# Optimization experiments

Measured on AMD Instinct MI355X. Metric: run time of the kernel, lower is better.

Reference implementation:

```python
import jax, jax.numpy as jnp
import numpy as np

IN_FEATURES = 1024
OUT_FEATURES = 64
KERNEL_DIMS = 16
N = 512


def setup_inputs() -> dict:
    key = jax.random.key(0)
    kx, kT = jax.random.split(key)
    x = jax.random.normal(kx, (N, IN_FEATURES), dtype=jnp.float32)
    T = jax.random.normal(kT, (IN_FEATURES, OUT_FEATURES, KERNEL_DIMS), dtype=jnp.float32)
    return {"x": x, "T": T}


def reference(x, T):
    n = x.shape[0]
    # Project: [N, in] @ [in, out*kd] -> [N, out, kd]
    matrices = (x @ T.reshape(T.shape[0], -1)).reshape(n, OUT_FEATURES, KERNEL_DIMS)
    # Pairwise L1 distance over kernel dims: [N, N, out]
    norm = jnp.abs(matrices[None, :, :, :] - matrices[:, None, :, :]).sum(axis=3)
    expnorm = jnp.exp(-norm)
    # Exclude self-similarity (diagonal) and sum over the batch axis
    mask = 1.0 - jnp.eye(n, dtype=x.dtype)
    o_b = (expnorm * mask[:, :, None]).sum(axis=1)  # [N, out]
    return jnp.concatenate([x, o_b], axis=1)
```

## Files before the change

### kernel.cpp

```cpp
#include <hip/hip_runtime.h>
#include <hip/hip_bf16.h>

#define NB     512
#define INF    1024
#define OUTF   64
#define KD     16
#define PROJ   (OUTF*KD)
#define OROW   (INF + OUTF)

typedef short short8 __attribute__((ext_vector_type(8)));
typedef float floatx4 __attribute__((ext_vector_type(4)));

__device__ __forceinline__ unsigned short f2bf(float f) {
    union { float f; unsigned u; } v; v.f = f;
    const unsigned u = v.u;
    return (unsigned short)((u + 0x7FFF + ((u >> 16) & 1)) >> 16);
}

__global__ __launch_bounds__(256) void copy_init(const float* __restrict__ x,
                                                 float* __restrict__ out) {
    const int row = blockIdx.x;
    const int t   = threadIdx.x;
    ((float4*)(out + (size_t)row * OROW))[t] =
        ((const float4*)(x + (size_t)row * INF))[t];
    if (t < 16) {
        ((float4*)(out + (size_t)row * OROW + INF))[t] =
            make_float4(-1.f, -1.f, -1.f, -1.f);
    }
}

#define LDT 40

__global__ __launch_bounds__(256) void gemm_mfma(const float* __restrict__ A,
                                                 const float* __restrict__ B,
                                                 float* __restrict__ C) {
    __shared__ short As[32 * LDT];
    __shared__ short Bs[64 * LDT];

    const int t    = threadIdx.x;
    const int lane = t & 63, w = t >> 6;
    const int bm = blockIdx.y * 32, bn = blockIdx.x * 64;
    const int mh = w & 1, nh = w >> 1;

    const int am = t >> 3, ak = (t & 7) * 4;
    const int bk = (t >> 4) * 2, bn0 = (t & 15) * 4;

    floatx4 acc0 = {0.f, 0.f, 0.f, 0.f};
    floatx4 acc1 = {0.f, 0.f, 0.f, 0.f};

    const int q = lane >> 4, c = lane & 15;
    const short* apf  = &As[(mh * 16 + c) * LDT + q * 8];
    const short* bpf0 = &Bs[(nh * 32 + c) * LDT + q * 8];
    const short* bpf1 = &Bs[(nh * 32 + 16 + c) * LDT + q * 8];

    for (int k0 = 0; k0 < INF; k0 += 32) {
        const float4 av  = *(const float4*)&A[(size_t)(bm + am) * INF + k0 + ak];
        const float4 bv0 = *(const float4*)&B[(size_t)(k0 + bk) * PROJ + bn + bn0];
        const float4 bv1 = *(const float4*)&B[(size_t)(k0 + bk + 1) * PROJ + bn + bn0];

        __syncthreads();
        const unsigned pa0 = f2bf(av.x) | ((unsigned)f2bf(av.y) << 16);
        const unsigned pa1 = f2bf(av.z) | ((unsigned)f2bf(av.w) << 16);
        *(uint2*)&As[am * LDT + ak] = make_uint2(pa0, pa1);
        *(unsigned*)&Bs[(bn0 + 0) * LDT + bk] = f2bf(bv0.x) | ((unsigned)f2bf(bv1.x) << 16);
        *(unsigned*)&Bs[(bn0 + 1) * LDT + bk] = f2bf(bv0.y) | ((unsigned)f2bf(bv1.y) << 16);
        *(unsigned*)&Bs[(bn0 + 2) * LDT + bk] = f2bf(bv0.z) | ((unsigned)f2bf(bv1.z) << 16);
        *(unsigned*)&Bs[(bn0 + 3) * LDT + bk] = f2bf(bv0.w) | ((unsigned)f2bf(bv1.w) << 16);
        __syncthreads();

        const short8 af  = *(const short8*)apf;
        const short8 bf0 = *(const short8*)bpf0;
        const short8 bf1 = *(const short8*)bpf1;
        acc0 = __builtin_amdgcn_mfma_f32_16x16x32_bf16(af, bf0, acc0, 0, 0, 0);
        acc1 = __builtin_amdgcn_mfma_f32_16x16x32_bf16(af, bf1, acc1, 0, 0, 0);
    }

#pragma unroll
    for (int r = 0; r < 4; ++r) {
        const int row = bm + mh * 16 + q * 4 + r;
        C[(size_t)row * PROJ + bn + nh * 32 + c]      = acc0[r];
        C[(size_t)row * PROJ + bn + nh * 32 + 16 + c] = acc1[r];
    }
}

__global__ __launch_bounds__(128) void pairwise_l1(const float* __restrict__ M,
                                                   float* __restrict__ out) {
    __shared__ float Mj[64 * 64];

    const int t  = threadIdx.x;
    const int o  = t & 3;
    const int il = t >> 2;
    const int og = blockIdx.x;
    const int ig = blockIdx.y;
    const int j0 = blockIdx.z * 64;
    const int i  = ig * 32 + il;

    const float4* myp = (const float4*)&M[(size_t)i * PROJ + og * 64 + o * 16];
    const float4 a0 = myp[0], a1 = myp[1], a2 = myp[2], a3 = myp[3];

#pragma unroll
    for (int cc = 0; cc < 8; ++cc) {
        const int idx = (cc * 128 + t) * 4;
        const int jl  = idx >> 6;
        const int col = idx & 63;
        *(float4*)&Mj[jl * 64 + col] =
            *(const float4*)&M[(size_t)(j0 + jl) * PROJ + og * 64 + col];
    }
    __syncthreads();

    float sum0 = 0.f, sum1 = 0.f;
#pragma unroll 4
    for (int jl = 0; jl < 64; ++jl) {
        const float4* bp = (const float4*)&Mj[jl * 64 + o * 16];
        const float4 b0 = bp[0], b1 = bp[1], b2 = bp[2], b3 = bp[3];
        float n0 = fabsf(a0.x - b0.x) + fabsf(a0.y - b0.y) +
                   fabsf(a0.z - b0.z) + fabsf(a0.w - b0.w);
        float n1 = fabsf(a1.x - b1.x) + fabsf(a1.y - b1.y) +
                   fabsf(a1.z - b1.z) + fabsf(a1.w - b1.w);
        float n2 = fabsf(a2.x - b2.x) + fabsf(a2.y - b2.y) +
                   fabsf(a2.z - b2.z) + fabsf(a2.w - b2.w);
        float n3 = fabsf(a3.x - b3.x) + fabsf(a3.y - b3.y) +
                   fabsf(a3.z - b3.z) + fabsf(a3.w - b3.w);
        const float norm = (n0 + n1) + (n2 + n3);
        if (jl & 1) sum1 += __expf(-norm);
        else        sum0 += __expf(-norm);
    }

    __hip_atomic_fetch_add(&out[(size_t)i * OROW + INF + og * 4 + o],
                           sum0 + sum1, __ATOMIC_RELAXED,
                           __HIP_MEMORY_SCOPE_AGENT);
}

extern "C" void kernel_launch(void* const* d_in, const int* in_sizes, int n_in,
                              void* d_out, int out_size, void* d_ws, size_t ws_size,
                              hipStream_t stream) {
    const float* x = (const float*)d_in[0];
    const float* T = (const float*)d_in[1];
    float* out = (float*)d_out;
    float* M   = (float*)d_ws;

    copy_init<<<dim3(NB), 256, 0, stream>>>(x, out);
    gemm_mfma<<<dim3(PROJ / 64, NB / 32), 256, 0, stream>>>(x, T, M);
    pairwise_l1<<<dim3(OUTF / 4, NB / 32, NB / 64), 128, 0, stream>>>(M, out);
}
```

Measured before the change: 101.1 us.

## Fuse copy-init into GEMM, store projection in fp16, use packed half2 L1

The output copy and -1 initialisation move into the GEMM kernel, removing one launch. The GEMM tile shrinks to 16 rows with one wave per 16 columns, and global loads are prefetched one iteration ahead. The projection is stored as fp16 and the pairwise kernel computes L1 distances with packed half2 arithmetic, which halves memory and LDS traffic and the ALU instruction count. The trade is lower precision in the distance sums, with a risk of fp16 overflow or accuracy loss.

```diff
diff --git a/kernel.cpp b/kernel.cpp
--- a/kernel.cpp
+++ b/kernel.cpp
@@ -1,91 +1,93 @@
 #include <hip/hip_runtime.h>
 #include <hip/hip_bf16.h>
+#include <hip/hip_fp16.h>
 
 #define NB     512
 #define INF    1024
 #define OUTF   64
-#define KD     16
-#define PROJ   (OUTF*KD)
+#define PROJ   1024
 #define OROW   (INF + OUTF)
 
 typedef short short8 __attribute__((ext_vector_type(8)));
 typedef float floatx4 __attribute__((ext_vector_type(4)));
 
-__device__ __forceinline__ unsigned short f2bf(float f) {
-    union { float f; unsigned u; } v; v.f = f;
-    const unsigned u = v.u;
-    return (unsigned short)((u + 0x7FFF + ((u >> 16) & 1)) >> 16);
+#define LDT 40
+
+__device__ __forceinline__ unsigned pack_bf16(float x, float y) {
+    __hip_bfloat162 h = __float22bfloat162_rn(make_float2(x, y));
+    union { __hip_bfloat162 h; unsigned u; } v; v.h = h; return v.u;
 }
 
-__global__ __launch_bounds__(256) void copy_init(const float* __restrict__ x,
-                                                 float* __restrict__ out) {
-    const int row = blockIdx.x;
-    const int t   = threadIdx.x;
-    ((float4*)(out + (size_t)row * OROW))[t] =
-        ((const float4*)(x + (size_t)row * INF))[t];
-    if (t < 16) {
-        ((float4*)(out + (size_t)row * OROW + INF))[t] =
-            make_float4(-1.f, -1.f, -1.f, -1.f);
-    }
+__device__ __forceinline__ __half2 as_h2(unsigned u) {
+    union { unsigned u; __half2 h; } v; v.u = u; return v.h;
 }
 
-#define LDT 40
-
-__global__ __launch_bounds__(256) void gemm_mfma(const float* __restrict__ A,
-                                                 const float* __restrict__ B,
-                                                 float* __restrict__ C) {
-    __shared__ short As[32 * LDT];
+__global__ __launch_bounds__(256, 2) void gemm_fused(const float* __restrict__ A,
+                                                     const float* __restrict__ B,
+                                                     float* __restrict__ out,
+                                                     __half* __restrict__ M16) {
+    __shared__ short As[16 * LDT];
     __shared__ short Bs[64 * LDT];
 
     const int t    = threadIdx.x;
     const int lane = t & 63, w = t >> 6;
-    const int bm = blockIdx.y * 32, bn = blockIdx.x * 64;
-    const int mh = w & 1, nh = w >> 1;
+    const int bnx = blockIdx.x, bmy = blockIdx.y;
+    const int bm = bmy * 16, bn = bnx * 64;
 
-    const int am = t >> 3, ak = (t & 7) * 4;
-    const int bk = (t >> 4) * 2, bn0 = (t & 15) * 4;
+    {
+        const int r = t >> 4, c4 = (t & 15) * 4;
+        *(float4*)&out[(size_t)(bm + r) * OROW + bn + c4] =
+            *(const float4*)&A[(size_t)(bm + r) * INF + bn + c4];
+    }
+    if (t < 16) {
+        const int row = bmy * 16 + bnx;
+        *(float4*)&out[(size_t)row * OROW + INF + t * 4] =
+            make_float4(-1.f, -1.f, -1.f, -1.f);
+    }
 
-    floatx4 acc0 = {0.f, 0.f, 0.f, 0.f};
-    floatx4 acc1 = {0.f, 0.f, 0.f, 0.f};
+    const int am = t >> 4,        ak  = (t & 15) * 2;
+    const int bk = (t >> 4) * 2,  bn0 = (t & 15) * 4;
 
     const int q = lane >> 4, c = lane & 15;
-    const short* apf  = &As[(mh * 16 + c) * LDT + q * 8];
-    const short* bpf0 = &Bs[(nh * 32 + c) * LDT + q * 8];
-    const short* bpf1 = &Bs[(nh * 32 + 16 + c) * LDT + q * 8];
+    const short* ap = &As[c * LDT + q * 8];
+    const short* bp = &Bs[(w * 16 + c) * LDT + q * 8];
+
+    floatx4 acc = {0.f, 0.f, 0.f, 0.f};
+
+    float2 av  = *(const float2*)&A[(size_t)(bm + am) * INF + ak];
+    float4 bv0 = *(const float4*)&B[(size_t)bk * PROJ + bn + bn0];
+    float4 bv1 = *(const float4*)&B[(size_t)(bk + 1) * PROJ + bn + bn0];
 
     for (int k0 = 0; k0 < INF; k0 += 32) {
-        const float4 av  = *(const float4*)&A[(size_t)(bm + am) * INF + k0 + ak];
-        const float4 bv0 = *(const float4*)&B[(size_t)(k0 + bk) * PROJ + bn + bn0];
-        const float4 bv1 = *(const float4*)&B[(size_t)(k0 + bk + 1) * PROJ + bn + bn0];
-
         __syncthreads();
-        const unsigned pa0 = f2bf(av.x) | ((unsigned)f2bf(av.y) << 16);
-        const unsigned pa1 = f2bf(av.z) | ((unsigned)f2bf(av.w) << 16);
-        *(uint2*)&As[am * LDT + ak] = make_uint2(pa0, pa1);
-        *(unsigned*)&Bs[(bn0 + 0) * LDT + bk] = f2bf(bv0.x) | ((unsigned)f2bf(bv1.x) << 16);
-        *(unsigned*)&Bs[(bn0 + 1) * LDT + bk] = f2bf(bv0.y) | ((unsigned)f2bf(bv1.y) << 16);
-        *(unsigned*)&Bs[(bn0 + 2) * LDT + bk] = f2bf(bv0.z) | ((unsigned)f2bf(bv1.z) << 16);
-        *(unsigned*)&Bs[(bn0 + 3) * LDT + bk] = f2bf(bv0.w) | ((unsigned)f2bf(bv1.w) << 16);
+        *(unsigned*)&As[am * LDT + ak]        = pack_bf16(av.x, av.y);
+        *(unsigned*)&Bs[(bn0 + 0) * LDT + bk] = pack_bf16(bv0.x, bv1.x);
+        *(unsigned*)&Bs[(bn0 + 1) * LDT + bk] = pack_bf16(bv0.y, bv1.y);
+        *(unsigned*)&Bs[(bn0 + 2) * LDT + bk] = pack_bf16(bv0.z, bv1.z);
+        *(unsigned*)&Bs[(bn0 + 3) * LDT + bk] = pack_bf16(bv0.w, bv1.w);
         __syncthreads();
 
-        const short8 af  = *(const short8*)apf;
-        const short8 bf0 = *(const short8*)bpf0;
-        const short8 bf1 = *(const short8*)bpf1;
-        acc0 = __builtin_amdgcn_mfma_f32_16x16x32_bf16(af, bf0, acc0, 0, 0, 0);
-        acc1 = __builtin_amdgcn_mfma_f32_16x16x32_bf16(af, bf1, acc1, 0, 0, 0);
+        const int kn = k0 + 32;
+        if (kn < INF) {
+            av  = *(const float2*)&A[(size_t)(bm + am) * INF + kn + ak];
+            bv0 = *(const float4*)&B[(size_t)(kn + bk) * PROJ + bn + bn0];
+            bv1 = *(const float4*)&B[(size_t)(kn + bk + 1) * PROJ + bn + bn0];
+        }
+
+        const short8 af = *(const short8*)ap;
+        const short8 bf = *(const short8*)bp;
+        acc = __builtin_amdgcn_mfma_f32_16x16x32_bf16(af, bf, acc, 0, 0, 0);
     }
 
 #pragma unroll
     for (int r = 0; r < 4; ++r) {
-        const int row = bm + mh * 16 + q * 4 + r;
-        C[(size_t)row * PROJ + bn + nh * 32 + c]      = acc0[r];
-        C[(size_t)row * PROJ + bn + nh * 32 + 16 + c] = acc1[r];
+        M16[(size_t)(bm + q * 4 + r) * PROJ + bn + w * 16 + c] = __float2half(acc[r]);
     }
 }
 
-__global__ __launch_bounds__(128) void pairwise_l1(const float* __restrict__ M,
+__global__ __launch_bounds__(128) void pairwise_h2(const __half* __restrict__ M16,
                                                    float* __restrict__ out) {
-    __shared__ float Mj[64 * 64];
+    __shared__ __half Mj[64 * 64];
 
     const int t  = threadIdx.x;
     const int o  = t & 3;
@@ -95,33 +97,34 @@
     const int j0 = blockIdx.z * 64;
     const int i  = ig * 32 + il;
 
-    const float4* myp = (const float4*)&M[(size_t)i * PROJ + og * 64 + o * 16];
-    const float4 a0 = myp[0], a1 = myp[1], a2 = myp[2], a3 = myp[3];
+    const uint4* mp = (const uint4*)&M16[(size_t)i * PROJ + og * 64 + o * 16];
+    const uint4 a0 = mp[0], a1 = mp[1];
 
 #pragma unroll
-    for (int cc = 0; cc < 8; ++cc) {
-        const int idx = (cc * 128 + t) * 4;
+    for (int cc = 0; cc < 4; ++cc) {
+        const int idx = (cc * 128 + t) * 8;
         const int jl  = idx >> 6;
         const int col = idx & 63;
-        *(float4*)&Mj[jl * 64 + col] =
-            *(const float4*)&M[(size_t)(j0 + jl) * PROJ + og * 64 + col];
+        *(uint4*)&Mj[jl * 64 + col] =
+            *(const uint4*)&M16[(size_t)(j0 + jl) * PROJ + og * 64 + col];
     }
     __syncthreads();
 
     float sum0 = 0.f, sum1 = 0.f;
 #pragma unroll 4
     for (int jl = 0; jl < 64; ++jl) {
-        const float4* bp = (const float4*)&Mj[jl * 64 + o * 16];
-        const float4 b0 = bp[0], b1 = bp[1], b2 = bp[2], b3 = bp[3];
-        float n0 = fabsf(a0.x - b0.x) + fabsf(a0.y - b0.y) +
-                   fabsf(a0.z - b0.z) + fabsf(a0.w - b0.w);
-        float n1 = fabsf(a1.x - b1.x) + fabsf(a1.y - b1.y) +
-                   fabsf(a1.z - b1.z) + fabsf(a1.w - b1.w);
-        float n2 = fabsf(a2.x - b2.x) + fabsf(a2.y - b2.y) +
-                   fabsf(a2.z - b2.z) + fabsf(a2.w - b2.w);
-        float n3 = fabsf(a3.x - b3.x) + fabsf(a3.y - b3.y) +
-                   fabsf(a3.z - b3.z) + fabsf(a3.w - b3.w);
-        const float norm = (n0 + n1) + (n2 + n3);
+        const uint4 b0 = *(const uint4*)&Mj[jl * 64 + o * 16];
+        const uint4 b1 = *(const uint4*)&Mj[jl * 64 + o * 16 + 8];
+        __half2 s0 = __hadd2(__habs2(__hsub2(as_h2(a0.x), as_h2(b0.x))),
+                             __habs2(__hsub2(as_h2(a0.y), as_h2(b0.y))));
+        __half2 s1 = __hadd2(__habs2(__hsub2(as_h2(a0.z), as_h2(b0.z))),
+                             __habs2(__hsub2(as_h2(a0.w), as_h2(b0.w))));
+        __half2 s2 = __hadd2(__habs2(__hsub2(as_h2(a1.x), as_h2(b1.x))),
+                             __habs2(__hsub2(as_h2(a1.y), as_h2(b1.y))));
+        __half2 s3 = __hadd2(__habs2(__hsub2(as_h2(a1.z), as_h2(b1.z))),
+                             __habs2(__hsub2(as_h2(a1.w), as_h2(b1.w))));
+        const __half2 s = __hadd2(__hadd2(s0, s1), __hadd2(s2, s3));
+        const float norm = __low2float(s) + __high2float(s);
         if (jl & 1) sum1 += __expf(-norm);
         else        sum0 += __expf(-norm);
     }
@@ -136,10 +139,9 @@
                               hipStream_t stream) {
     const float* x = (const float*)d_in[0];
     const float* T = (const float*)d_in[1];
-    float* out = (float*)d_out;
-    float* M   = (float*)d_ws;
+    float* out  = (float*)d_out;
+    __half* M16 = (__half*)d_ws;
 
-    copy_init<<<dim3(NB), 256, 0, stream>>>(x, out);
-    gemm_mfma<<<dim3(PROJ / 64, NB / 32), 256, 0, stream>>>(x, T, M);
-    pairwise_l1<<<dim3(OUTF / 4, NB / 32, NB / 64), 128, 0, stream>>>(M, out);
+    gemm_fused<<<dim3(PROJ / 64, NB / 16), 256, 0, stream>>>(x, T, out, M16);
+    pairwise_h2<<<dim3(OUTF / 4, NB / 32, NB / 64), 128, 0, stream>>>(M16, out);
 }
```

Result: faster. 92.92 us (-8.1%).
